# Kernel optimization log

Hardware: AMD Instinct MI355X
Metric: run time of the kernel (lower is better)

## Reference

```python
import jax, jax.numpy as jnp
import numpy as np
import math

N_HEAD = 16
N_CTX = 1024


def setup_inputs() -> dict:
    key = jax.random.key(0)
    ks = jax.random.split(key, 3)
    B, S, NX = 4, 1024, 1024
    x = jax.random.normal(ks[0], (B, S, NX), dtype=jnp.float32)
    # Conv1D weights stored as [nx, nf], init std=0.02, bias zeros
    c_attn_w = jax.random.normal(ks[1], (NX, 3 * NX), dtype=jnp.float32) * 0.02
    c_attn_b = jnp.zeros((3 * NX,), dtype=jnp.float32)
    c_proj_w = jax.random.normal(ks[2], (NX, NX), dtype=jnp.float32) * 0.02
    c_proj_b = jnp.zeros((NX,), dtype=jnp.float32)
    return {"x": x, "c_attn_w": c_attn_w, "c_attn_b": c_attn_b,
            "c_proj_w": c_proj_w, "c_proj_b": c_proj_b}


def reference(x, c_attn_w, c_attn_b, c_proj_w, c_proj_b):
    B, S, NX = x.shape
    H = N_HEAD
    D = NX // H
    # c_attn: Conv1D -> x @ W + b, then split into q, k, v
    qkv = x @ c_attn_w + c_attn_b                      # [B,S,3*NX]
    q, k, v = jnp.split(qkv, 3, axis=-1)               # each [B,S,NX]
    # split heads: q,v -> [B,H,S,D]; k -> [B,H,D,S]
    q = q.reshape(B, S, H, D).transpose(0, 2, 1, 3)
    k = k.reshape(B, S, H, D).transpose(0, 2, 3, 1)
    v = v.reshape(B, S, H, D).transpose(0, 2, 1, 3)
    # _attn: scores, scale, combined multiplicative+additive causal mask, softmax
    w = jnp.matmul(q, k)                               # [B,H,S,S]
    w = w / math.sqrt(D)                               # scale=True
    bias = jnp.tril(jnp.ones((S, S), dtype=w.dtype))[None, None]  # causal tril slice
    w = w * bias - 1e10 * (1.0 - bias)
    w = jax.nn.softmax(w, axis=-1)
    a = jnp.matmul(w, v)                               # [B,H,S,D]
    # merge heads
    a = a.transpose(0, 2, 1, 3).reshape(B, S, NX)
    # c_proj
    return a @ c_proj_w + c_proj_b
```

## Files before the change

### kernel.cpp

```cpp
#include <hip/hip_runtime.h>
#include <cstdint>

typedef __attribute__((ext_vector_type(8))) short short8;
typedef __attribute__((ext_vector_type(4))) short short4x;
typedef __attribute__((ext_vector_type(4))) float floatx4;

__device__ __forceinline__ unsigned short f2b(float f) {
    unsigned int u = __builtin_bit_cast(unsigned int, f);
    u += 0x7fffu + ((u >> 16) & 1u);
    return (unsigned short)(u >> 16);
}
__device__ __forceinline__ float b2f(unsigned short s) {
    unsigned int u = ((unsigned int)s) << 16;
    return __builtin_bit_cast(float, u);
}
__device__ __forceinline__ float fast_exp2(float x) {
    float r;
    asm("v_exp_f32 %0, %1" : "=v"(r) : "v"(x));
    return r;
}
__device__ __forceinline__ unsigned int pack_bf16_trunc(float lo, float hi) {
    return __builtin_amdgcn_perm(__builtin_bit_cast(unsigned int, hi),
                                 __builtin_bit_cast(unsigned int, lo), 0x07060302u);
}

#define GLDS(g, l) __builtin_amdgcn_global_load_lds(                                   \
    (const __attribute__((address_space(1))) unsigned int*)(g),                        \
    (__attribute__((address_space(3))) unsigned int*)(l), 16, 0, 0)

__global__ __launch_bounds__(256) void prep_kernel(const float* __restrict__ x,
                                                   unsigned short* __restrict__ xb,
                                                   const float* __restrict__ w1,
                                                   unsigned short* __restrict__ w1t,
                                                   const float* __restrict__ w2,
                                                   unsigned short* __restrict__ w2t) {
    __shared__ unsigned short tile[64][65];
    const int b = blockIdx.x, t = threadIdx.x;
    if (b < 1024) {
        for (int i = b * 256 + t; i < 1048576; i += 262144) {
            float4 v = ((const float4*)x)[i];
            ushort4 o;
            o.x = f2b(v.x); o.y = f2b(v.y); o.z = f2b(v.z); o.w = f2b(v.w);
            ((ushort4*)xb)[i] = o;
        }
        return;
    }
    const float* W; unsigned short* Wt; int K, N, kb, nb;
    if (b < 1792) { W = w1; Wt = w1t; K = 1024; N = 3072; kb = (b - 1024) & 15; nb = (b - 1024) >> 4; }
    else          { W = w2; Wt = w2t; K = 1024; N = 1024; kb = (b - 1792) & 15; nb = (b - 1792) >> 4; }
    const int k0 = kb * 64, n0 = nb * 64;
    for (int idx = t; idx < 64 * 64; idx += 256) {
        int i = idx >> 6, j = idx & 63;
        tile[j][i] = f2b(W[(size_t)(k0 + i) * N + n0 + j]);
    }
    __syncthreads();
    for (int idx = t; idx < 64 * 64; idx += 256) {
        int r = idx >> 6, c = idx & 63;
        Wt[(size_t)(n0 + r) * K + k0 + c] = tile[r][c];
    }
}

#define MFMA16(a_, b_, c_) __builtin_amdgcn_mfma_f32_16x16x32_bf16((a_), (b_), (c_), 0, 0, 0)

#define PH12(m0) do {                                              \
    acc[(m0)][0]     = MFMA16(a00, b00, acc[(m0)][0]);             \
    acc[(m0) + 1][0] = MFMA16(a10, b00, acc[(m0) + 1][0]);         \
    acc[(m0)][1]     = MFMA16(a00, b10, acc[(m0)][1]);             \
    acc[(m0) + 1][1] = MFMA16(a10, b10, acc[(m0) + 1][1]);         \
    acc[(m0)][2]     = MFMA16(a00, b20, acc[(m0)][2]);             \
    acc[(m0) + 1][2] = MFMA16(a10, b20, acc[(m0) + 1][2]);         \
    acc[(m0)][0]     = MFMA16(a01, b01, acc[(m0)][0]);             \
    acc[(m0) + 1][0] = MFMA16(a11, b01, acc[(m0) + 1][0]);         \
    acc[(m0)][1]     = MFMA16(a01, b11, acc[(m0)][1]);             \
    acc[(m0) + 1][1] = MFMA16(a11, b11, acc[(m0) + 1][1]);         \
    acc[(m0)][2]     = MFMA16(a01, b21, acc[(m0)][2]);             \
    acc[(m0) + 1][2] = MFMA16(a11, b21, acc[(m0) + 1][2]);         \
} while (0)

#define LDA(mi, kc) (*(const short8*)&As[buf][aRow + (mi) * 1024 + ((kc) ? g1 : g0)])
#define LDB(ni, kc) (*(const short8*)&Bs[buf][bRow + (ni) * 1024 + ((kc) ? g1 : g0)])

#define STAGE_A02(kt_) { const unsigned short* s_ = aSrc + (kt_) * 64;  \
    GLDS(s_,             &As[(kt_) & 1][ldsOff]);                       \
    GLDS(s_ + 128 * 1024, &As[(kt_) & 1][8192 + ldsOff]); }
#define STAGE_A13(kt_) { const unsigned short* s_ = aSrc + (kt_) * 64;  \
    GLDS(s_ + 64 * 1024,  &As[(kt_) & 1][4096 + ldsOff]);               \
    GLDS(s_ + 192 * 1024, &As[(kt_) & 1][12288 + ldsOff]); }
#define STAGE_B3(kt_) { const unsigned short* s_ = bSrc + (kt_) * 64;   \
    GLDS(s_,             &Bs[(kt_) & 1][ldsOff]);                       \
    GLDS(s_ + 64 * 1024,  &Bs[(kt_) & 1][4096 + ldsOff]);               \
    GLDS(s_ + 128 * 1024, &Bs[(kt_) & 1][8192 + ldsOff]); }

__global__ __launch_bounds__(512, 2) void gemm_bt_kernel(const unsigned short* __restrict__ A,
                                                         const unsigned short* __restrict__ Bt,
                                                         const float* __restrict__ bias,
                                                         unsigned short* __restrict__ C,
                                                         unsigned short* __restrict__ vTout,
                                                         int vSplit) {
    __shared__ unsigned short As[2][256 * 64];
    __shared__ unsigned short Bs[2][192 * 64];

    const int t = threadIdx.x;
    const int wave = t >> 6, lane = t & 63;
    const int quad = lane >> 4, l16 = lane & 15;
    const int wm = wave >> 2, wn = wave & 3;
    const int rowBase = blockIdx.x << 8;
    const int colBase = blockIdx.y * 192;

    floatx4 acc[8][3];
#pragma unroll
    for (int i = 0; i < 8; ++i)
#pragma unroll
        for (int j = 0; j < 3; ++j) acc[i][j] = (floatx4){0.f, 0.f, 0.f, 0.f};

    const int rr = t >> 3;
    const int gsrc = ((t & 7) ^ (rr & 7)) * 8;
    const unsigned short* aSrc = A + (size_t)(rowBase + rr) * 1024 + gsrc;
    const unsigned short* bSrc = Bt + (size_t)(colBase + rr) * 1024 + gsrc;
    const int ldsOff = t * 8;

    const int rg = l16 & 7;
    const int g0 = (quad ^ rg) * 8;
    const int g1 = g0 ^ 32;
    const int aRow = (wm * 128 + l16) * 64;
    const int bRow = (wn * 48 + l16) * 64;

    STAGE_B3(0); STAGE_A02(0); STAGE_A13(0); STAGE_B3(1); STAGE_A02(1);
    asm volatile("s_waitcnt vmcnt(7)" ::: "memory");
    __builtin_amdgcn_s_barrier();

    for (int kt = 0; kt < 14; ++kt) {
        const int buf = kt & 1;
        short8 b00, b01, b10, b11, b20, b21;
#pragma unroll
        for (int p = 0; p < 4; ++p) {
            if (p == 0) {
                b00 = LDB(0, 0); b01 = LDB(0, 1);
                b10 = LDB(1, 0); b11 = LDB(1, 1);
                b20 = LDB(2, 0); b21 = LDB(2, 1);
            }
            short8 a00 = LDA(2 * p, 0),     a01 = LDA(2 * p, 1);
            short8 a10 = LDA(2 * p + 1, 0), a11 = LDA(2 * p + 1, 1);
            if (p == 0) STAGE_A13(kt + 1);
            if (p == 1) STAGE_B3(kt + 2);
            if (p == 2) STAGE_A02(kt + 2);
            if (p == 1) asm volatile("s_waitcnt vmcnt(10)" ::: "memory");
            if (p == 3) asm volatile("s_waitcnt vmcnt(7)" ::: "memory");
            __builtin_amdgcn_s_barrier();
            asm volatile("s_waitcnt lgkmcnt(0)" ::: "memory");
            __builtin_amdgcn_s_setprio(1);
            PH12(2 * p);
            __builtin_amdgcn_s_setprio(0);
            __builtin_amdgcn_s_barrier();
        }
    }

    STAGE_A13(15);
    asm volatile("s_waitcnt vmcnt(0)" ::: "memory");
    __builtin_amdgcn_s_barrier();
#pragma unroll
    for (int kt2 = 14; kt2 < 16; ++kt2) {
        const int buf = kt2 & 1;
        short8 b00 = LDB(0, 0), b01 = LDB(0, 1);
        short8 b10 = LDB(1, 0), b11 = LDB(1, 1);
        short8 b20 = LDB(2, 0), b21 = LDB(2, 1);
#pragma unroll
        for (int m0 = 0; m0 < 8; m0 += 2) {
            short8 a00 = LDA(m0, 0),     a01 = LDA(m0, 1);
            short8 a10 = LDA(m0 + 1, 0), a11 = LDA(m0 + 1, 1);
            PH12(m0);
        }
    }

#pragma unroll
    for (int mi = 0; mi < 8; ++mi) {
        const int row0 = rowBase + wm * 128 + mi * 16 + quad * 4;
#pragma unroll
        for (int ni = 0; ni < 3; ++ni) {
            const int colA = colBase + wn * 48 + ni * 16 + l16;
            const float bv = bias[colA];
            if (colA >= vSplit) {
                const int vcol = colA - vSplit;
#pragma unroll
                for (int r = 0; r < 4; ++r) {
                    const int row = row0 + r;
                    vTout[((size_t)((row >> 10) * 16 + (vcol >> 6)) * 64 + (vcol & 63)) * 1024
                          + (row & 1023)] = f2b(acc[mi][ni][r] + bv);
                }
            } else {
#pragma unroll
                for (int r = 0; r < 4; ++r) {
                    const int row = row0 + r;
                    C[(size_t)row * 3072 + colA] = f2b(acc[mi][ni][r] + bv);
                }
            }
        }
    }
}

#define G2LDA(mi, kc) (*(const short8*)&As2[buf][aRow + (mi) * 1024 + ((kc) ? g1 : g0)])
#define G2LDB(ni, kc) (*(const short8*)&Bs2[buf][bRow + (ni) * 1024 + ((kc) ? g1 : g0)])
#define G2STAGE(kt_) { const unsigned short* sa_ = aSrc + (kt_) * 64;   \
    const unsigned short* sb_ = bSrc + (kt_) * 64;                      \
    GLDS(sa_,              &As2[(kt_) & 1][ldsOff]);                    \
    GLDS(sa_ + 64 * 1024,  &As2[(kt_) & 1][4096 + ldsOff]);             \
    GLDS(sb_,              &Bs2[(kt_) & 1][ldsOff]);                    \
    GLDS(sb_ + 64 * 1024,  &Bs2[(kt_) & 1][4096 + ldsOff]); }

__global__ __launch_bounds__(512, 2) void gemm2_kernel(const unsigned short* __restrict__ A,
                                                       const unsigned short* __restrict__ Bt,
                                                       const float* __restrict__ bias,
                                                       float* __restrict__ C) {
    __shared__ unsigned short As2[2][128 * 64];
    __shared__ unsigned short Bs2[2][128 * 64];

    const int t = threadIdx.x;
    const int wave = t >> 6, lane = t & 63;
    const int quad = lane >> 4, l16 = lane & 15;
    const int wm = wave >> 2, wn = wave & 3;
    const int rowBase = blockIdx.x << 7;
    const int colBase = blockIdx.y << 7;

    floatx4 acc[4][2];
#pragma unroll
    for (int i = 0; i < 4; ++i)
#pragma unroll
        for (int j = 0; j < 2; ++j) acc[i][j] = (floatx4){0.f, 0.f, 0.f, 0.f};

    const int rr = t >> 3;
    const int gsrc = ((t & 7) ^ (rr & 7)) * 8;
    const unsigned short* aSrc = A + (size_t)(rowBase + rr) * 1024 + gsrc;
    const unsigned short* bSrc = Bt + (size_t)(colBase + rr) * 1024 + gsrc;
    const int ldsOff = t * 8;

    const int rg = l16 & 7;
    const int g0 = (quad ^ rg) * 8;
    const int g1 = g0 ^ 32;
    const int aRow = (wm * 64 + l16) * 64;
    const int bRow = (wn * 32 + l16) * 64;

    G2STAGE(0);

    for (int kt = 0; kt < 16; ++kt) {
        const int buf = kt & 1;
        asm volatile("s_waitcnt vmcnt(0)" ::: "memory");
        __builtin_amdgcn_s_barrier();
        if (kt + 1 < 16) G2STAGE(kt + 1);

        short8 a0k0 = G2LDA(0, 0), a0k1 = G2LDA(0, 1);
        short8 a1k0 = G2LDA(1, 0), a1k1 = G2LDA(1, 1);
        short8 a2k0 = G2LDA(2, 0), a2k1 = G2LDA(2, 1);
        short8 a3k0 = G2LDA(3, 0), a3k1 = G2LDA(3, 1);
        short8 b0k0 = G2LDB(0, 0), b0k1 = G2LDB(0, 1);
        short8 b1k0 = G2LDB(1, 0), b1k1 = G2LDB(1, 1);
        asm volatile("s_waitcnt lgkmcnt(0)" ::: "memory");
        __builtin_amdgcn_sched_barrier(0);
        __builtin_amdgcn_s_setprio(1);
        acc[0][0] = MFMA16(a0k0, b0k0, acc[0][0]);
        acc[1][0] = MFMA16(a1k0, b0k0, acc[1][0]);
        acc[2][0] = MFMA16(a2k0, b0k0, acc[2][0]);
        acc[3][0] = MFMA16(a3k0, b0k0, acc[3][0]);
        acc[0][1] = MFMA16(a0k0, b1k0, acc[0][1]);
        acc[1][1] = MFMA16(a1k0, b1k0, acc[1][1]);
        acc[2][1] = MFMA16(a2k0, b1k0, acc[2][1]);
        acc[3][1] = MFMA16(a3k0, b1k0, acc[3][1]);
        acc[0][0] = MFMA16(a0k1, b0k1, acc[0][0]);
        acc[1][0] = MFMA16(a1k1, b0k1, acc[1][0]);
        acc[2][0] = MFMA16(a2k1, b0k1, acc[2][0]);
        acc[3][0] = MFMA16(a3k1, b0k1, acc[3][0]);
        acc[0][1] = MFMA16(a0k1, b1k1, acc[0][1]);
        acc[1][1] = MFMA16(a1k1, b1k1, acc[1][1]);
        acc[2][1] = MFMA16(a2k1, b1k1, acc[2][1]);
        acc[3][1] = MFMA16(a3k1, b1k1, acc[3][1]);
        __builtin_amdgcn_s_setprio(0);
    }

#pragma unroll
    for (int mi = 0; mi < 4; ++mi)
#pragma unroll
        for (int ni = 0; ni < 2; ++ni) {
            int col = colBase + wn * 32 + ni * 16 + l16;
            float bv = bias[col];
#pragma unroll
            for (int r = 0; r < 4; ++r) {
                int row = rowBase + wm * 64 + mi * 16 + quad * 4 + r;
                C[(size_t)row * 1024 + col] = acc[mi][ni][r] + bv;
            }
        }
}

__global__ __launch_bounds__(256) void attn_kernel(const unsigned short* __restrict__ qkv,
                                                   const unsigned short* __restrict__ vT,
                                                   unsigned short* __restrict__ aout) {
    __shared__ unsigned short Ks[2][2][4096];
    __shared__ unsigned short Vs[2][2][4096];
    __shared__ unsigned short Tb[4][16 * 72];

    const int p  = blockIdx.x;
    const int bh = blockIdx.y;
    const int b = bh >> 4, h = bh & 15;
    const int qb1 = p, qb2 = 15 - p;
    const int t = threadIdx.x;
    const int wave = t >> 6, lane = t & 63;
    const int quad = lane >> 4, l16 = lane & 15;
    const int h7 = l16 & 7;

    const size_t rowB = (size_t)b * 1024;
    const size_t hoff = (size_t)h * 64;
    const int qA0 = qb1 * 64 + wave * 16;
    const int qB0 = qb2 * 64 + wave * 16;

    const float qscale = 0.125f * 1.44269504f;
    short8 qfA[2], qfB[2];
#pragma unroll
    for (int kc = 0; kc < 2; ++kc) {
        short8 qa = *(const short8*)(qkv + (rowB + qA0 + l16) * 3072 + hoff + kc * 32 + quad * 8);
        short8 qb = *(const short8*)(qkv + (rowB + qB0 + l16) * 3072 + hoff + kc * 32 + quad * 8);
#pragma unroll
        for (int e = 0; e < 8; ++e) {
            qa[e] = (short)f2b(b2f((unsigned short)qa[e]) * qscale);
            qb[e] = (short)f2b(b2f((unsigned short)qb[e]) * qscale);
        }
        qfA[kc] = qa; qfB[kc] = qb;
    }

    const int lr = lane >> 3;
    const int sc8 = (lane & 7) * 8;
    const int gc8 = ((lane & 7) ^ lr) * 8;
    const unsigned short* kSrc = qkv + rowB * 3072 + hoff + 1024;
    const unsigned short* vSrc = vT + (size_t)bh * 65536;

    auto stageT = [&](int kt, int bf, int sl) {
        const unsigned short* kp = kSrc + (size_t)kt * 64 * 3072;
        const unsigned short* vp = vSrc + kt * 64;
        int r0 = wave * 16 + lr, r1 = r0 + 8;
        GLDS(kp + (size_t)r0 * 3072 + gc8, &Ks[bf][sl][r0 * 64 + sc8]);
        GLDS(kp + (size_t)r1 * 3072 + gc8, &Ks[bf][sl][r1 * 64 + sc8]);
        GLDS(vp + (size_t)r0 * 1024 + gc8, &Vs[bf][sl][r0 * 64 + sc8]);
        GLDS(vp + (size_t)r1 * 1024 + gc8, &Vs[bf][sl][r1 * 64 + sc8]);
    };

    float lpA = 0.f, lpB = 0.f;
    floatx4 oA[4], oB[4];
#pragma unroll
    for (int ni = 0; ni < 4; ++ni) {
        oA[ni] = (floatx4){0.f, 0.f, 0.f, 0.f};
        oB[ni] = (floatx4){0.f, 0.f, 0.f, 0.f};
    }

    const int nT = qb2 + 1;
    const int nP = (nT + 1) >> 1;

    auto doTile = [&](int kt, const unsigned short* Kb, const unsigned short* Vb) {
        short8 kf[4][2];
#pragma unroll
        for (int jn = 0; jn < 4; ++jn)
#pragma unroll
            for (int kc = 0; kc < 2; ++kc)
                kf[jn][kc] = *(const short8*)&Kb[(jn * 16 + l16) * 64 + (((kc * 4 + quad) ^ h7) * 8)];
        short4x vf[4][4];
#pragma unroll
        for (int ni = 0; ni < 4; ++ni)
#pragma unroll
            for (int jb = 0; jb < 4; ++jb)
                vf[ni][jb] = *(const short4x*)&Vb[(ni * 16 + l16) * 64 +
                                                 (((jb * 2 + (quad >> 1)) ^ h7) * 8) + (quad & 1) * 4];

        auto qtile = [&](short8 (&qf)[2], floatx4 (&o)[4], float& lp, bool diag) {
            floatx4 s[4];
#pragma unroll
            for (int jn = 0; jn < 4; ++jn) s[jn] = (floatx4){0.f, 0.f, 0.f, 0.f};
#pragma unroll
            for (int jn = 0; jn < 4; ++jn)
#pragma unroll
                for (int kc = 0; kc < 2; ++kc)
                    s[jn] = __builtin_amdgcn_mfma_f32_16x16x32_bf16(kf[jn][kc], qf[kc], s[jn], 0, 0, 0);
            if (diag) {
                int ql = wave * 16 + l16;
#pragma unroll
                for (int jn = 0; jn < 4; ++jn)
#pragma unroll
                    for (int r = 0; r < 4; ++r)
                        if (jn * 16 + quad * 4 + r > ql) s[jn][r] = -1e30f;
            }
            short4x pb[4];
#pragma unroll
            for (int jb = 0; jb < 4; ++jb) {
                float pe0 = fast_exp2(s[jb][0]);
                float pe1 = fast_exp2(s[jb][1]);
                float pe2 = fast_exp2(s[jb][2]);
                float pe3 = fast_exp2(s[jb][3]);
                lp += (pe0 + pe1) + (pe2 + pe3);
                uint2 u;
                u.x = pack_bf16_trunc(pe0, pe1);
                u.y = pack_bf16_trunc(pe2, pe3);
                pb[jb] = __builtin_bit_cast(short4x, u);
            }
#pragma unroll
            for (int jb = 0; jb < 4; ++jb)
#pragma unroll
                for (int ni = 0; ni < 4; ++ni)
                    o[ni] = __builtin_amdgcn_mfma_f32_16x16x16bf16_1k(vf[ni][jb], pb[jb], o[ni], 0, 0, 0);
        };

        qtile(qfB, oB, lpB, kt == qb2);
        if (kt <= qb1) qtile(qfA, oA, lpA, kt == qb1);
    };

    stageT(0, 0, 0);
    stageT(1, 0, 1);

    for (int pi = 0; pi < nP; ++pi) {
        __syncthreads();
        if (pi + 1 < nP) {
            stageT(2 * pi + 2, (pi + 1) & 1, 0);
            if (2 * pi + 3 < nT) stageT(2 * pi + 3, (pi + 1) & 1, 1);
        }
        const int bfI = pi & 1;
        doTile(2 * pi, &Ks[bfI][0][0], &Vs[bfI][0][0]);
        if (2 * pi + 1 < nT) doTile(2 * pi + 1, &Ks[bfI][1][0], &Vs[bfI][1][0]);
    }

    lpA += __shfl_xor(lpA, 16); lpA += __shfl_xor(lpA, 32);
    lpB += __shfl_xor(lpB, 16); lpB += __shfl_xor(lpB, 32);
    const float liA = 1.f / lpA, liB = 1.f / lpB;

    auto writeOut = [&](floatx4 (&o)[4], float li, int q0) {
#pragma unroll
        for (int ni = 0; ni < 4; ++ni)
#pragma unroll
            for (int r = 0; r < 4; ++r)
                Tb[wave][l16 * 72 + ni * 16 + quad * 4 + r] = f2b(o[ni][r] * li);
#pragma unroll
        for (int i = 0; i < 2; ++i) {
            int q = lane >> 2, c = (lane & 3) + 4 * i;
            short8 v = *(const short8*)&Tb[wave][q * 72 + c * 8];
            *(short8*)(aout + (rowB + q0 + q) * 1024 + hoff + c * 8) = v;
        }
    };
    writeOut(oA, liA, qA0);
    writeOut(oB, liB, qB0);
}

extern "C" void kernel_launch(void* const* d_in, const int* in_sizes, int n_in,
                              void* d_out, int out_size, void* d_ws, size_t ws_size,
                              hipStream_t stream) {
    const float* x  = (const float*)d_in[0];
    const float* w1 = (const float*)d_in[1];
    const float* b1 = (const float*)d_in[2];
    const float* w2 = (const float*)d_in[3];
    const float* b2 = (const float*)d_in[4];
    float* out = (float*)d_out;

    unsigned short* xb   = (unsigned short*)d_ws;
    unsigned short* w1t  = xb  + (size_t)4096 * 1024;
    unsigned short* w2t  = w1t + (size_t)3072 * 1024;
    unsigned short* qkv  = w2t + (size_t)1024 * 1024;
    unsigned short* attn = qkv + (size_t)4096 * 3072;
    unsigned short* vTb  = attn + (size_t)4096 * 1024;

    prep_kernel<<<2048, 256, 0, stream>>>(x, xb, w1, w1t, w2, w2t);
    gemm_bt_kernel<<<dim3(16, 16), 512, 0, stream>>>(xb, w1t, b1, qkv, vTb, 2048);
    attn_kernel<<<dim3(8, 64), 256, 0, stream>>>(qkv, vTb, attn);
    gemm2_kernel<<<dim3(32, 8), 512, 0, stream>>>(attn, w2t, b2, out);
}
```

Before: 165.3 us.

## Replace 256x192 pipelined QKV GEMM with simpler 128x128 tile, 4-wave kernel

Rewrites the QKV projection GEMM to use 128x128 output tiles, 256 threads with a 2x2 wave layout, and a plain double-buffered loop that waits for all loads each k-step. The deep hand-scheduled 512-thread pipeline with staggered staging and partial vmcnt waits is removed. The grid grows from 256 to 768 blocks, giving better balance across CUs, but the larger block count lowers per-block data reuse. The full vmcnt(0) wait each iteration may also expose more memory latency.

```diff
diff --git a/kernel.cpp b/kernel.cpp
--- a/kernel.cpp
+++ b/kernel.cpp
@@ -62,56 +62,42 @@
 
 #define MFMA16(a_, b_, c_) __builtin_amdgcn_mfma_f32_16x16x32_bf16((a_), (b_), (c_), 0, 0, 0)
 
-#define PH12(m0) do {                                              \
-    acc[(m0)][0]     = MFMA16(a00, b00, acc[(m0)][0]);             \
-    acc[(m0) + 1][0] = MFMA16(a10, b00, acc[(m0) + 1][0]);         \
-    acc[(m0)][1]     = MFMA16(a00, b10, acc[(m0)][1]);             \
-    acc[(m0) + 1][1] = MFMA16(a10, b10, acc[(m0) + 1][1]);         \
-    acc[(m0)][2]     = MFMA16(a00, b20, acc[(m0)][2]);             \
-    acc[(m0) + 1][2] = MFMA16(a10, b20, acc[(m0) + 1][2]);         \
-    acc[(m0)][0]     = MFMA16(a01, b01, acc[(m0)][0]);             \
-    acc[(m0) + 1][0] = MFMA16(a11, b01, acc[(m0) + 1][0]);         \
-    acc[(m0)][1]     = MFMA16(a01, b11, acc[(m0)][1]);             \
-    acc[(m0) + 1][1] = MFMA16(a11, b11, acc[(m0) + 1][1]);         \
-    acc[(m0)][2]     = MFMA16(a01, b21, acc[(m0)][2]);             \
-    acc[(m0) + 1][2] = MFMA16(a11, b21, acc[(m0) + 1][2]);         \
-} while (0)
-
-#define LDA(mi, kc) (*(const short8*)&As[buf][aRow + (mi) * 1024 + ((kc) ? g1 : g0)])
-#define LDB(ni, kc) (*(const short8*)&Bs[buf][bRow + (ni) * 1024 + ((kc) ? g1 : g0)])
-
-#define STAGE_A02(kt_) { const unsigned short* s_ = aSrc + (kt_) * 64;  \
-    GLDS(s_,             &As[(kt_) & 1][ldsOff]);                       \
-    GLDS(s_ + 128 * 1024, &As[(kt_) & 1][8192 + ldsOff]); }
-#define STAGE_A13(kt_) { const unsigned short* s_ = aSrc + (kt_) * 64;  \
-    GLDS(s_ + 64 * 1024,  &As[(kt_) & 1][4096 + ldsOff]);               \
-    GLDS(s_ + 192 * 1024, &As[(kt_) & 1][12288 + ldsOff]); }
-#define STAGE_B3(kt_) { const unsigned short* s_ = bSrc + (kt_) * 64;   \
-    GLDS(s_,             &Bs[(kt_) & 1][ldsOff]);                       \
-    GLDS(s_ + 64 * 1024,  &Bs[(kt_) & 1][4096 + ldsOff]);               \
-    GLDS(s_ + 128 * 1024, &Bs[(kt_) & 1][8192 + ldsOff]); }
-
-__global__ __launch_bounds__(512, 2) void gemm_bt_kernel(const unsigned short* __restrict__ A,
-                                                         const unsigned short* __restrict__ Bt,
-                                                         const float* __restrict__ bias,
-                                                         unsigned short* __restrict__ C,
-                                                         unsigned short* __restrict__ vTout,
-                                                         int vSplit) {
-    __shared__ unsigned short As[2][256 * 64];
-    __shared__ unsigned short Bs[2][192 * 64];
+#define GBLDA(mi, kc) (*(const short8*)&As[buf][aRow + (mi) * 1024 + ((kc) ? g1 : g0)])
+#define GBLDB(ni, kc) (*(const short8*)&Bs[buf][bRow + (ni) * 1024 + ((kc) ? g1 : g0)])
+#define GBSTAGE(kt_) {                                                  \
+    const unsigned short* sa_ = aSrc + (kt_) * 64;                      \
+    const unsigned short* sb_ = bSrc + (kt_) * 64;                      \
+    GLDS(sa_,              &As[(kt_) & 1][ldsOff]);                     \
+    GLDS(sa_ + 32 * 1024,  &As[(kt_) & 1][2048 + ldsOff]);              \
+    GLDS(sa_ + 64 * 1024,  &As[(kt_) & 1][4096 + ldsOff]);              \
+    GLDS(sa_ + 96 * 1024,  &As[(kt_) & 1][6144 + ldsOff]);              \
+    GLDS(sb_,              &Bs[(kt_) & 1][ldsOff]);                     \
+    GLDS(sb_ + 32 * 1024,  &Bs[(kt_) & 1][2048 + ldsOff]);              \
+    GLDS(sb_ + 64 * 1024,  &Bs[(kt_) & 1][4096 + ldsOff]);              \
+    GLDS(sb_ + 96 * 1024,  &Bs[(kt_) & 1][6144 + ldsOff]); }
+
+__global__ __launch_bounds__(256) void gemm_bt_kernel(const unsigned short* __restrict__ A,
+                                                      const unsigned short* __restrict__ Bt,
+                                                      const float* __restrict__ bias,
+                                                      unsigned short* __restrict__ C,
+                                                      unsigned short* __restrict__ vTout,
+                                                      int vSplit) {
+    __shared__ unsigned short As[2][128 * 64];
+    __shared__ unsigned short Bs[2][128 * 64];
 
     const int t = threadIdx.x;
     const int wave = t >> 6, lane = t & 63;
     const int quad = lane >> 4, l16 = lane & 15;
-    const int wm = wave >> 2, wn = wave & 3;
-    const int rowBase = blockIdx.x << 8;
-    const int colBase = blockIdx.y * 192;
-
-    floatx4 acc[8][3];
-#pragma unroll
-    for (int i = 0; i < 8; ++i)
-#pragma unroll
-        for (int j = 0; j < 3; ++j) acc[i][j] = (floatx4){0.f, 0.f, 0.f, 0.f};
+    const int rowBase = blockIdx.x << 7;
+    const int colBase = blockIdx.y << 7;
+    const int waveM = (wave >> 1) * 64;
+    const int waveN = (wave & 1) * 64;
+
+    floatx4 acc[4][4];
+#pragma unroll
+    for (int i = 0; i < 4; ++i)
+#pragma unroll
+        for (int j = 0; j < 4; ++j) acc[i][j] = (floatx4){0.f, 0.f, 0.f, 0.f};
 
     const int rr = t >> 3;
     const int gsrc = ((t & 7) ^ (rr & 7)) * 8;
@@ -122,79 +108,66 @@
     const int rg = l16 & 7;
     const int g0 = (quad ^ rg) * 8;
     const int g1 = g0 ^ 32;
-    const int aRow = (wm * 128 + l16) * 64;
-    const int bRow = (wn * 48 + l16) * 64;
-
-    STAGE_B3(0); STAGE_A02(0); STAGE_A13(0); STAGE_B3(1); STAGE_A02(1);
-    asm volatile("s_waitcnt vmcnt(7)" ::: "memory");
-    __builtin_amdgcn_s_barrier();
-
-    for (int kt = 0; kt < 14; ++kt) {
+    const int aRow = (waveM + l16) * 64;
+    const int bRow = (waveN + l16) * 64;
+
+    GBSTAGE(0);
+
+    for (int kt = 0; kt < 16; ++kt) {
         const int buf = kt & 1;
-        short8 b00, b01, b10, b11, b20, b21;
-#pragma unroll
-        for (int p = 0; p < 4; ++p) {
-            if (p == 0) {
-                b00 = LDB(0, 0); b01 = LDB(0, 1);
-                b10 = LDB(1, 0); b11 = LDB(1, 1);
-                b20 = LDB(2, 0); b21 = LDB(2, 1);
-            }
-            short8 a00 = LDA(2 * p, 0),     a01 = LDA(2 * p, 1);
-            short8 a10 = LDA(2 * p + 1, 0), a11 = LDA(2 * p + 1, 1);
-            if (p == 0) STAGE_A13(kt + 1);
-            if (p == 1) STAGE_B3(kt + 2);
-            if (p == 2) STAGE_A02(kt + 2);
-            if (p == 1) asm volatile("s_waitcnt vmcnt(10)" ::: "memory");
-            if (p == 3) asm volatile("s_waitcnt vmcnt(7)" ::: "memory");
-            __builtin_amdgcn_s_barrier();
-            asm volatile("s_waitcnt lgkmcnt(0)" ::: "memory");
-            __builtin_amdgcn_s_setprio(1);
-            PH12(2 * p);
-            __builtin_amdgcn_s_setprio(0);
-            __builtin_amdgcn_s_barrier();
-        }
-    }
-
-    STAGE_A13(15);
-    asm volatile("s_waitcnt vmcnt(0)" ::: "memory");
-    __builtin_amdgcn_s_barrier();
-#pragma unroll
-    for (int kt2 = 14; kt2 < 16; ++kt2) {
-        const int buf = kt2 & 1;
-        short8 b00 = LDB(0, 0), b01 = LDB(0, 1);
-        short8 b10 = LDB(1, 0), b11 = LDB(1, 1);
-        short8 b20 = LDB(2, 0), b21 = LDB(2, 1);
-#pragma unroll
-        for (int m0 = 0; m0 < 8; m0 += 2) {
-            short8 a00 = LDA(m0, 0),     a01 = LDA(m0, 1);
-            short8 a10 = LDA(m0 + 1, 0), a11 = LDA(m0 + 1, 1);
-            PH12(m0);
-        }
-    }
-
-#pragma unroll
-    for (int mi = 0; mi < 8; ++mi) {
-        const int row0 = rowBase + wm * 128 + mi * 16 + quad * 4;
-#pragma unroll
-        for (int ni = 0; ni < 3; ++ni) {
-            const int colA = colBase + wn * 48 + ni * 16 + l16;
-            const float bv = bias[colA];
-            if (colA >= vSplit) {
-                const int vcol = colA - vSplit;
+        asm volatile("s_waitcnt vmcnt(0)" ::: "memory");
+        __builtin_amdgcn_s_barrier();
+        if (kt + 1 < 16) GBSTAGE(kt + 1);
+
+        short8 af[4][2], bf[4][2];
+#pragma unroll
+        for (int mi = 0; mi < 4; ++mi) {
+            af[mi][0] = GBLDA(mi, 0); af[mi][1] = GBLDA(mi, 1);
+        }
+#pragma unroll
+        for (int ni = 0; ni < 4; ++ni) {
+            bf[ni][0] = GBLDB(ni, 0); bf[ni][1] = GBLDB(ni, 1);
+        }
+        asm volatile("s_waitcnt lgkmcnt(0)" ::: "memory");
+        __builtin_amdgcn_sched_barrier(0);
+        __builtin_amdgcn_s_setprio(1);
+#pragma unroll
+        for (int kc = 0; kc < 2; ++kc)
+#pragma unroll
+            for (int mi = 0; mi < 4; ++mi)
+#pragma unroll
+                for (int ni = 0; ni < 4; ++ni)
+                    acc[mi][ni] = MFMA16(af[mi][kc], bf[ni][kc], acc[mi][ni]);
+        __builtin_amdgcn_s_setprio(0);
+    }
+
+    if (colBase >= vSplit) {
+#pragma unroll
+        for (int mi = 0; mi < 4; ++mi)
+#pragma unroll
+            for (int ni = 0; ni < 4; ++ni) {
+                int col = colBase + waveN + ni * 16 + l16 - vSplit;
+                float bv = bias[colBase + waveN + ni * 16 + l16];
 #pragma unroll
                 for (int r = 0; r < 4; ++r) {
-                    const int row = row0 + r;
-                    vTout[((size_t)((row >> 10) * 16 + (vcol >> 6)) * 64 + (vcol & 63)) * 1024
+                    int row = rowBase + waveM + mi * 16 + quad * 4 + r;
+                    vTout[((size_t)((row >> 10) * 16 + (col >> 6)) * 64 + (col & 63)) * 1024
                           + (row & 1023)] = f2b(acc[mi][ni][r] + bv);
                 }
-            } else {
+            }
+    } else {
+#pragma unroll
+        for (int mi = 0; mi < 4; ++mi)
+#pragma unroll
+            for (int ni = 0; ni < 4; ++ni) {
+                int col = colBase + waveN + ni * 16 + l16;
+                float bv = bias[col];
 #pragma unroll
                 for (int r = 0; r < 4; ++r) {
-                    const int row = row0 + r;
-                    C[(size_t)row * 3072 + colA] = f2b(acc[mi][ni][r] + bv);
+                    int row = rowBase + waveM + mi * 16 + quad * 4 + r;
+                    C[(size_t)row * 3072 + col] = f2b(acc[mi][ni][r] + bv);
                 }
             }
-        }
     }
 }
 
@@ -460,7 +433,7 @@
     unsigned short* vTb  = attn + (size_t)4096 * 1024;
 
     prep_kernel<<<2048, 256, 0, stream>>>(x, xb, w1, w1t, w2, w2t);
-    gemm_bt_kernel<<<dim3(16, 16), 512, 0, stream>>>(xb, w1t, b1, qkv, vTb, 2048);
+    gemm_bt_kernel<<<dim3(32, 24), 256, 0, stream>>>(xb, w1t, b1, qkv, vTb, 2048);
     attn_kernel<<<dim3(8, 64), 256, 0, stream>>>(qkv, vTb, attn);
     gemm2_kernel<<<dim3(32, 8), 512, 0, stream>>>(attn, w2t, b2, out);
 }
```

Result: slower. 174.2 us (+5.4%).
